# Optimization experiments

Measured on AMD Instinct MI355X. Metric: run time of the kernel, lower is better.

## Reference

```python
import jax
jax.config.update("jax_enable_x64", True)
import jax.numpy as jnp
import numpy as np

CKA_WEIGHT = 0.1


def _group_cka_sum(feats):
    """feats: [F, N, D] float. Returns sum of pairwise CKA over all (i,j) pairs.

    Faithful to CKASR: K = X X^T with zeroed diagonal, unbiased HSIC
    (Song et al. estimator), CKA[i,j] = HSIC(Ki,Kj)/sqrt(HSIC(Ki,Ki)HSIC(Kj,Kj)).
    All pairwise loops are batched into einsums.
    """
    F, N, D = feats.shape
    X = feats.reshape(F, N, D).astype(jnp.float64)
    K = jnp.einsum('fnd,fmd->fnm', X, X)                 # [F,N,N] Gram
    K = K * (1.0 - jnp.eye(N, dtype=K.dtype))            # fill_diagonal_(0)
    # HSIC(Ki, Kj) = 1/(N(N-3)) * ( tr(Ki Kj)
    #   + sum(Ki) sum(Kj) / ((N-1)(N-2))
    #   - 2/(N-2) * <rowsum(Ki), rowsum(Kj)> )
    trKL = jnp.einsum('iab,jab->ij', K, K)               # tr(Ki Kj), K symmetric
    s = jnp.sum(K, axis=(1, 2))                          # [F] total sums
    r = jnp.sum(K, axis=2)                               # [F,N] row sums
    rr = jnp.einsum('ia,ja->ij', r, r)                   # [F,F]
    hsic = (trKL + jnp.outer(s, s) / ((N - 1) * (N - 2))
            - 2.0 * rr / (N - 2)) / (N * (N - 3))        # [F,F]
    d = jnp.sqrt(jnp.diagonal(hsic))                     # [F]
    cka = hsic / (d[:, None] * d[None, :])
    return jnp.sum(cka)


def setup_inputs() -> dict:
    key = jax.random.key(0)
    k1, k2, k3, k4 = jax.random.split(key, 4)
    N, C = 64, 1000
    output = jax.random.normal(k1, (N, C), dtype=jnp.float32)
    target = jax.random.randint(k2, (N,), 0, C, dtype=jnp.int64)
    feats_a = jax.random.normal(k3, (3, N, 65536), dtype=jnp.float32)
    feats_b = jax.random.normal(k4, (4, N, 32768), dtype=jnp.float32)
    return {"output": output, "target": target,
            "feats_a": feats_a, "feats_b": feats_b}


def reference(output, target, feats_a, feats_b):
    N = output.shape[0]
    logp = jax.nn.log_softmax(output.astype(jnp.float32), axis=-1)
    ce = -jnp.mean(logp[jnp.arange(N), target])           # CrossEntropyLoss (mean)
    cka = _group_cka_sum(feats_a) + _group_cka_sum(feats_b)
    loss = ce + CKA_WEIGHT * cka.astype(jnp.float32)
    return (loss, output)
```

## Files before the change

### kernel.cpp

```cpp
#include <hip/hip_runtime.h>
#include <hip/hip_bf16.h>
#include <math.h>

typedef __attribute__((ext_vector_type(8))) short short8;
typedef __attribute__((ext_vector_type(4))) float f32x4;

#define PSTRIDE 4160

__device__ __forceinline__ unsigned int bf16_rn(float x) {
    unsigned int u = __float_as_uint(x);
    return (u + 0x7FFFu + ((u >> 16) & 1u)) >> 16;
}

__global__ __launch_bounds__(256) void ce_kernel(
    const float* __restrict__ logits, const int* __restrict__ target,
    float* __restrict__ out_copy, float* __restrict__ ce_rows)
{
    const int row = blockIdx.x;
    const float* x = logits + row * 1000;
    const int t = threadIdx.x;
    __shared__ float red[256];

    float m = -INFINITY;
    for (int i = t; i < 1000; i += 256) {
        float v = x[i];
        out_copy[row * 1000 + i] = v;
        m = fmaxf(m, v);
    }
    red[t] = m; __syncthreads();
    for (int s = 128; s > 0; s >>= 1) {
        if (t < s) red[t] = fmaxf(red[t], red[t + s]);
        __syncthreads();
    }
    m = red[0];
    __syncthreads();

    float ssum = 0.f;
    for (int i = t; i < 1000; i += 256) ssum += expf(x[i] - m);
    red[t] = ssum; __syncthreads();
    for (int s = 128; s > 0; s >>= 1) {
        if (t < s) red[t] += red[t + s];
        __syncthreads();
    }
    if (t == 0) {
        double lse = (double)m + log((double)red[0]);
        int tg = target[row];
        ce_rows[row] = (float)(-((double)x[tg] - lse));
    }
}

__global__ __launch_bounds__(256) void gramf_kernel(
    const float* __restrict__ A, const float* __restrict__ B,
    float* __restrict__ partials, int nfA, int nfB)
{
    __shared__ f32x4 ldsv[4096];
    char* lds = (char*)ldsv;

    const int blk = blockIdx.x;
    const int uA = nfA * 128;
    const float* xf;
    int c, D;
    if (blk < uA) {
        int f = blk >> 7; c = blk & 127; D = 65536;
        xf = A + (size_t)f * 64 * 65536;
    } else {
        int v = blk - uA;
        int f = v >> 6; c = v & 63; D = 32768;
        xf = B + (size_t)f * 64 * 32768;
    }

    const int t = threadIdx.x;
    const int wave = t >> 6, lane = t & 63;
    const int k0 = c * 512;

#pragma unroll 4
    for (int rr = 0; rr < 16; ++rr) {
        const int row = wave * 16 + rr;
        const float* p = xf + (size_t)row * D + k0 + lane * 8;
        float4 va = *(const float4*)p;
        float4 vb = *(const float4*)(p + 4);
        float vv[8] = {va.x, va.y, va.z, va.w, vb.x, vb.y, vb.z, vb.w};
        short8 hv;
#pragma unroll
        for (int j = 0; j < 8; ++j) hv[j] = (short)bf16_rn(vv[j]);
        const int boff = (lane * 16) ^ ((row & 7) << 4);
        *(short8*)(lds + row * 1024 + boff) = hv;
    }
    __syncthreads();

    const int m = lane & 15, quad = lane >> 4;
    const int loff = wave * 256 + quad * 16;

    f32x4 acc[4][4];
#pragma unroll
    for (int i = 0; i < 4; ++i)
#pragma unroll
        for (int j = 0; j < 4; ++j) acc[i][j] = (f32x4)0.f;

    short8 fr[4][4];
#pragma unroll
    for (int s = 0; s < 4; ++s)
#pragma unroll
        for (int tm = 0; tm < 4; ++tm) {
            const int row = tm * 16 + m;
            const int boff = (loff + s * 64) ^ ((row & 7) << 4);
            fr[s][tm] = *(const short8*)(lds + row * 1024 + boff);
        }
#pragma unroll
    for (int s = 0; s < 4; ++s)
#pragma unroll
        for (int tm = 0; tm < 4; ++tm)
#pragma unroll
            for (int tn = 0; tn < 4; ++tn)
                acc[tm][tn] = __builtin_amdgcn_mfma_f32_16x16x32_bf16(
                    fr[s][tm], fr[s][tn], acc[tm][tn], 0, 0, 0);

    __syncthreads();
    float* kbuf = (float*)lds;
    if (wave == 0) {
#pragma unroll
        for (int tm = 0; tm < 4; ++tm)
#pragma unroll
            for (int tn = 0; tn < 4; ++tn)
#pragma unroll
                for (int r = 0; r < 4; ++r)
                    kbuf[(tm * 16 + quad * 4 + r) * 64 + tn * 16 + m] = acc[tm][tn][r];
    }
    __syncthreads();
    if (wave != 0) {
#pragma unroll
        for (int tm = 0; tm < 4; ++tm)
#pragma unroll
            for (int tn = 0; tn < 4; ++tn)
#pragma unroll
                for (int r = 0; r < 4; ++r)
                    atomicAdd(&kbuf[(tm * 16 + quad * 4 + r) * 64 + tn * 16 + m],
                              acc[tm][tn][r]);
    }
    __syncthreads();

    float4* outp = (float4*)(partials + (size_t)blk * PSTRIDE);
    const float4* kb4 = (const float4*)kbuf;
    for (int e = t; e < 1024; e += 256) outp[e] = kb4[e];
}

__global__ __launch_bounds__(256) void reduce_kernel(
    const float* __restrict__ partials, float* __restrict__ K, int singleF)
{
    __shared__ double red[256];
    int f, eblk, base, count;
    if (singleF < 0) {
        f = blockIdx.x >> 6; eblk = blockIdx.x & 63;
        if (f < 3) { base = f * 128;            count = 128; }
        else       { base = 384 + (f - 3) * 64; count = 64;  }
    } else {
        f = singleF; eblk = blockIdx.x; base = 0;
        count = (f < 3) ? 128 : 64;
    }
    const int e = (eblk << 6) + (threadIdx.x & 63);
    const int jg = threadIdx.x >> 6;

    double s0 = 0.0, s1 = 0.0;
    for (int j = jg; j < count; j += 8) {
        s0 += (double)partials[(size_t)(base + j) * PSTRIDE + e];
        s1 += (double)partials[(size_t)(base + j + 4) * PSTRIDE + e];
    }
    red[threadIdx.x] = s0 + s1;
    __syncthreads();
    if (jg == 0) {
        double tot = red[threadIdx.x] + red[threadIdx.x + 64]
                   + red[threadIdx.x + 128] + red[threadIdx.x + 192];
        int rr = e >> 6, cc = e & 63;
        K[f * 4096 + e] = (rr == cc) ? 0.f : (float)tot;
    }
}

__global__ __launch_bounds__(256) void hsic_kernel(
    const float* __restrict__ K, double* __restrict__ hsic_out)
{
    const int p = blockIdx.x;
    int i, j;
    if (p < 9) { i = p / 3; j = p % 3; }
    else       { int q = p - 9; i = 3 + q / 4; j = 3 + q % 4; }
    const float* Ki = K + i * 4096;
    const float* Kj = K + j * 4096;
    const int t = threadIdx.x;

    __shared__ double red[256];
    __shared__ double ri[64], rj[64];

    double local = 0.0;
    for (int e = t; e < 4096; e += 256)
        local += (double)Ki[e] * (double)Kj[e];
    red[t] = local; __syncthreads();
    for (int s = 128; s > 0; s >>= 1) {
        if (t < s) red[t] += red[t + s];
        __syncthreads();
    }

    if (t < 64) {
        double s = 0.0;
        for (int mc = 0; mc < 64; ++mc) s += (double)Ki[t * 64 + mc];
        ri[t] = s;
    } else if (t < 128) {
        int n = t - 64;
        double s = 0.0;
        for (int mc = 0; mc < 64; ++mc) s += (double)Kj[n * 64 + mc];
        rj[n] = s;
    }
    __syncthreads();

    if (t == 0) {
        double tr = red[0];
        double rr = 0.0, si = 0.0, sj = 0.0;
        for (int n = 0; n < 64; ++n) {
            rr += ri[n] * rj[n];
            si += ri[n];
            sj += rj[n];
        }
        const double N = 64.0;
        const double c1 = (N - 1.0) * (N - 2.0);
        const double c2 = N - 2.0;
        const double c3 = N * (N - 3.0);
        hsic_out[p] = (tr + si * sj / c1 - 2.0 * rr / c2) / c3;
    }
}

__global__ __launch_bounds__(64) void final_kernel(
    const double* __restrict__ hsic, const float* __restrict__ ce_rows,
    float* __restrict__ out_loss)
{
    if (threadIdx.x != 0) return;
    double ce = 0.0;
    for (int n = 0; n < 64; ++n) ce += (double)ce_rows[n];
    ce /= 64.0;

    double cka_total = 0.0;
    for (int i = 0; i < 3; ++i)
        for (int j = 0; j < 3; ++j)
            cka_total += hsic[i * 3 + j] / sqrt(hsic[i * 3 + i] * hsic[j * 3 + j]);
    for (int i = 0; i < 4; ++i)
        for (int j = 0; j < 4; ++j)
            cka_total += hsic[9 + i * 4 + j] / sqrt(hsic[9 + i * 4 + i] * hsic[9 + j * 4 + j]);

    out_loss[0] = (float)(ce + 0.1 * cka_total);
}

extern "C" void kernel_launch(void* const* d_in, const int* in_sizes, int n_in,
                              void* d_out, int out_size, void* d_ws, size_t ws_size,
                              hipStream_t stream)
{
    const float* output  = (const float*)d_in[0];
    const int*   target  = (const int*)d_in[1];
    const float* feats_a = (const float*)d_in[2];
    const float* feats_b = (const float*)d_in[3];
    float* out = (float*)d_out;

    char* ws = (char*)d_ws;
    float*  K       = (float*)ws;
    float*  ce_rows = (float*)(ws + 114688);
    double* hsic    = (double*)(ws + 114944);
    float*  partials = (float*)(ws + 131072);

    const size_t partMain = (size_t)640 * PSTRIDE * 4;
    const size_t mainNeed = 131072 + partMain;

    hipLaunchKernelGGL(ce_kernel, dim3(64), dim3(256), 0, stream,
                       output, target, out + 1, ce_rows);

    if (ws_size >= mainNeed) {
        hipLaunchKernelGGL(gramf_kernel, dim3(640), dim3(256), 0, stream,
                           feats_a, feats_b, partials, 3, 4);
        hipLaunchKernelGGL(reduce_kernel, dim3(448), dim3(256), 0, stream,
                           partials, K, -1);
    } else {
        for (int f = 0; f < 7; ++f) {
            if (f < 3) {
                const float* X = feats_a + (size_t)f * 64 * 65536;
                hipLaunchKernelGGL(gramf_kernel, dim3(128), dim3(256), 0, stream,
                                   X, (const float*)nullptr, partials, 1, 0);
            } else {
                const float* X = feats_b + (size_t)(f - 3) * 64 * 32768;
                hipLaunchKernelGGL(gramf_kernel, dim3(64), dim3(256), 0, stream,
                                   (const float*)nullptr, X, partials, 0, 1);
            }
            hipLaunchKernelGGL(reduce_kernel, dim3(64), dim3(256), 0, stream,
                               partials, K, f);
        }
    }

    hipLaunchKernelGGL(hsic_kernel, dim3(25), dim3(256), 0, stream, K, hsic);
    hipLaunchKernelGGL(final_kernel, dim3(1), dim3(64), 0, stream,
                       hsic, ce_rows, out);
}
```

Before: 182.1 us.

## Fuse CE into gram kernel, drop LDS staging, merge HSIC and final kernels

```diff
diff --git a/kernel.cpp b/kernel.cpp
--- a/kernel.cpp
+++ b/kernel.cpp
@@ -1,9 +1,9 @@
 #include <hip/hip_runtime.h>
-#include <hip/hip_bf16.h>
 #include <math.h>
 
 typedef __attribute__((ext_vector_type(8))) short short8;
 typedef __attribute__((ext_vector_type(4))) float f32x4;
+typedef __attribute__((ext_vector_type(16))) float f32x16;
 
 #define PSTRIDE 4160
 
@@ -12,136 +12,124 @@
     return (u + 0x7FFFu + ((u >> 16) & 1u)) >> 16;
 }
 
-__global__ __launch_bounds__(256) void ce_kernel(
+__device__ __forceinline__ short8 cvt8(float4 a, float4 b) {
+    short8 h;
+    h[0] = (short)bf16_rn(a.x); h[1] = (short)bf16_rn(a.y);
+    h[2] = (short)bf16_rn(a.z); h[3] = (short)bf16_rn(a.w);
+    h[4] = (short)bf16_rn(b.x); h[5] = (short)bf16_rn(b.y);
+    h[6] = (short)bf16_rn(b.z); h[7] = (short)bf16_rn(b.w);
+    return h;
+}
+
+__global__ __launch_bounds__(512, 6) void gram_ce_kernel(
+    const float* __restrict__ A, const float* __restrict__ B,
+    float* __restrict__ partials, int nfA, int nfB,
     const float* __restrict__ logits, const int* __restrict__ target,
-    float* __restrict__ out_copy, float* __restrict__ ce_rows)
-{
-    const int row = blockIdx.x;
-    const float* x = logits + row * 1000;
+    float* __restrict__ out_copy, float* __restrict__ ce_rows, int ceCount)
+{
+    __shared__ float smem[4096];
     const int t = threadIdx.x;
-    __shared__ float red[256];
-
-    float m = -INFINITY;
-    for (int i = t; i < 1000; i += 256) {
-        float v = x[i];
-        out_copy[row * 1000 + i] = v;
-        m = fmaxf(m, v);
-    }
-    red[t] = m; __syncthreads();
-    for (int s = 128; s > 0; s >>= 1) {
-        if (t < s) red[t] = fmaxf(red[t], red[t + s]);
-        __syncthreads();
-    }
-    m = red[0];
-    __syncthreads();
-
-    float ssum = 0.f;
-    for (int i = t; i < 1000; i += 256) ssum += expf(x[i] - m);
-    red[t] = ssum; __syncthreads();
-    for (int s = 128; s > 0; s >>= 1) {
-        if (t < s) red[t] += red[t + s];
-        __syncthreads();
-    }
-    if (t == 0) {
-        double lse = (double)m + log((double)red[0]);
-        int tg = target[row];
-        ce_rows[row] = (float)(-((double)x[tg] - lse));
-    }
-}
-
-__global__ __launch_bounds__(256) void gramf_kernel(
-    const float* __restrict__ A, const float* __restrict__ B,
-    float* __restrict__ partials, int nfA, int nfB)
-{
-    __shared__ f32x4 ldsv[4096];
-    char* lds = (char*)ldsv;
-
-    const int blk = blockIdx.x;
+
+    if ((int)blockIdx.x < ceCount) {
+        const int row = blockIdx.x;
+        const float* x = logits + row * 1000;
+        float m = -INFINITY;
+        for (int i = t; i < 1000; i += 512) {
+            float v = x[i];
+            out_copy[row * 1000 + i] = v;
+            m = fmaxf(m, v);
+        }
+        smem[t] = m; __syncthreads();
+        for (int s = 256; s > 0; s >>= 1) {
+            if (t < s) smem[t] = fmaxf(smem[t], smem[t + s]);
+            __syncthreads();
+        }
+        m = smem[0];
+        __syncthreads();
+        float ssum = 0.f;
+        for (int i = t; i < 1000; i += 512) ssum += expf(x[i] - m);
+        smem[t] = ssum; __syncthreads();
+        for (int s = 256; s > 0; s >>= 1) {
+            if (t < s) smem[t] += smem[t + s];
+            __syncthreads();
+        }
+        if (t == 0) {
+            double lse = (double)m + log((double)smem[0]);
+            int tg = target[row];
+            ce_rows[row] = (float)(-((double)x[tg] - lse));
+        }
+        return;
+    }
+
+    const int gb = blockIdx.x - ceCount;
     const int uA = nfA * 128;
     const float* xf;
     int c, D;
-    if (blk < uA) {
-        int f = blk >> 7; c = blk & 127; D = 65536;
+    if (gb < uA) {
+        int f = gb >> 7; c = gb & 127; D = 65536;
         xf = A + (size_t)f * 64 * 65536;
     } else {
-        int v = blk - uA;
+        int v = gb - uA;
         int f = v >> 6; c = v & 63; D = 32768;
         xf = B + (size_t)f * 64 * 32768;
     }
 
-    const int t = threadIdx.x;
     const int wave = t >> 6, lane = t & 63;
-    const int k0 = c * 512;
-
-#pragma unroll 4
-    for (int rr = 0; rr < 16; ++rr) {
-        const int row = wave * 16 + rr;
-        const float* p = xf + (size_t)row * D + k0 + lane * 8;
-        float4 va = *(const float4*)p;
-        float4 vb = *(const float4*)(p + 4);
-        float vv[8] = {va.x, va.y, va.z, va.w, vb.x, vb.y, vb.z, vb.w};
-        short8 hv;
-#pragma unroll
-        for (int j = 0; j < 8; ++j) hv[j] = (short)bf16_rn(vv[j]);
-        const int boff = (lane * 16) ^ ((row & 7) << 4);
-        *(short8*)(lds + row * 1024 + boff) = hv;
-    }
-    __syncthreads();
-
-    const int m = lane & 15, quad = lane >> 4;
-    const int loff = wave * 256 + quad * 16;
-
-    f32x4 acc[4][4];
-#pragma unroll
-    for (int i = 0; i < 4; ++i)
-#pragma unroll
-        for (int j = 0; j < 4; ++j) acc[i][j] = (f32x4)0.f;
-
-    short8 fr[4][4];
-#pragma unroll
-    for (int s = 0; s < 4; ++s)
-#pragma unroll
-        for (int tm = 0; tm < 4; ++tm) {
-            const int row = tm * 16 + m;
-            const int boff = (loff + s * 64) ^ ((row & 7) << 4);
-            fr[s][tm] = *(const short8*)(lds + row * 1024 + boff);
-        }
-#pragma unroll
-    for (int s = 0; s < 4; ++s)
-#pragma unroll
-        for (int tm = 0; tm < 4; ++tm)
-#pragma unroll
-            for (int tn = 0; tn < 4; ++tn)
-                acc[tm][tn] = __builtin_amdgcn_mfma_f32_16x16x32_bf16(
-                    fr[s][tm], fr[s][tn], acc[tm][tn], 0, 0, 0);
-
-    __syncthreads();
-    float* kbuf = (float*)lds;
-    if (wave == 0) {
-#pragma unroll
-        for (int tm = 0; tm < 4; ++tm)
-#pragma unroll
-            for (int tn = 0; tn < 4; ++tn)
-#pragma unroll
-                for (int r = 0; r < 4; ++r)
-                    kbuf[(tm * 16 + quad * 4 + r) * 64 + tn * 16 + m] = acc[tm][tn][r];
-    }
-    __syncthreads();
-    if (wave != 0) {
-#pragma unroll
-        for (int tm = 0; tm < 4; ++tm)
-#pragma unroll
-            for (int tn = 0; tn < 4; ++tn)
-#pragma unroll
-                for (int r = 0; r < 4; ++r)
-                    atomicAdd(&kbuf[(tm * 16 + quad * 4 + r) * 64 + tn * 16 + m],
-                              acc[tm][tn][r]);
-    }
-    __syncthreads();
-
-    float4* outp = (float4*)(partials + (size_t)blk * PSTRIDE);
-    const float4* kb4 = (const float4*)kbuf;
-    for (int e = t; e < 1024; e += 256) outp[e] = kb4[e];
+    const int q = wave & 3, h = wave >> 2;
+    const int wr = q >> 1, wc = q & 1;
+    const int lr = lane & 31, hi = lane >> 5;
+    const int k0 = c * 512 + h * 256 + hi * 8;
+
+    const float* pA = xf + (size_t)(wr * 32 + lr) * D + k0;
+    const float* pB = xf + (size_t)(wc * 32 + lr) * D + k0;
+
+    f32x16 acc = (f32x16)0.f;
+    if (wr == wc) {
+#pragma unroll
+        for (int s = 0; s < 16; ++s) {
+            float4 a0 = *(const float4*)(pA + s * 16);
+            float4 a1 = *(const float4*)(pA + s * 16 + 4);
+            short8 fa = cvt8(a0, a1);
+            acc = __builtin_amdgcn_mfma_f32_32x32x16_bf16(fa, fa, acc, 0, 0, 0);
+        }
+    } else {
+#pragma unroll
+        for (int s = 0; s < 16; ++s) {
+            float4 a0 = *(const float4*)(pA + s * 16);
+            float4 a1 = *(const float4*)(pA + s * 16 + 4);
+            float4 b0 = *(const float4*)(pB + s * 16);
+            float4 b1 = *(const float4*)(pB + s * 16 + 4);
+            short8 fa = cvt8(a0, a1);
+            short8 fb = cvt8(b0, b1);
+            acc = __builtin_amdgcn_mfma_f32_32x32x16_bf16(fa, fb, acc, 0, 0, 0);
+        }
+    }
+
+    float* qb = smem + q * 1024;
+    if (h == 0) {
+#pragma unroll
+        for (int r = 0; r < 16; ++r) {
+            int rl = (r & 3) + 8 * (r >> 2) + 4 * hi;
+            qb[rl * 32 + lr] = acc[r];
+        }
+    }
+    __syncthreads();
+    if (h == 1) {
+#pragma unroll
+        for (int r = 0; r < 16; ++r) {
+            int rl = (r & 3) + 8 * (r >> 2) + 4 * hi;
+            qb[rl * 32 + lr] += acc[r];
+        }
+    }
+    __syncthreads();
+
+    float* outp = partials + (size_t)gb * PSTRIDE;
+    const f32x4* s4 = (const f32x4*)smem;
+    f32x4* o4 = (f32x4*)outp;
+    for (int e = t; e < 1024; e += 512) {
+        int qq = e >> 8, rl = (e >> 3) & 31, cl = e & 7;
+        o4[((qq >> 1) * 32 + rl) * 16 + (qq & 1) * 8 + cl] = s4[e];
+    }
 }
 
 __global__ __launch_bounds__(256) void reduce_kernel(
@@ -175,75 +163,73 @@
     }
 }
 
-__global__ __launch_bounds__(256) void hsic_kernel(
-    const float* __restrict__ K, double* __restrict__ hsic_out)
-{
-    const int p = blockIdx.x;
-    int i, j;
-    if (p < 9) { i = p / 3; j = p % 3; }
-    else       { int q = p - 9; i = 3 + q / 4; j = 3 + q % 4; }
-    const float* Ki = K + i * 4096;
-    const float* Kj = K + j * 4096;
+__global__ __launch_bounds__(256) void cka_final_kernel(
+    const float* __restrict__ K, const float* __restrict__ ce_rows,
+    float* __restrict__ out_loss)
+{
+    __shared__ double rs[448];
+    __shared__ double sf[8];
+    __shared__ double red[256];
+    __shared__ double hs[25];
     const int t = threadIdx.x;
 
-    __shared__ double red[256];
-    __shared__ double ri[64], rj[64];
-
-    double local = 0.0;
-    for (int e = t; e < 4096; e += 256)
-        local += (double)Ki[e] * (double)Kj[e];
-    red[t] = local; __syncthreads();
-    for (int s = 128; s > 0; s >>= 1) {
-        if (t < s) red[t] += red[t + s];
-        __syncthreads();
-    }
-
-    if (t < 64) {
+    for (int g = t; g < 448; g += 256) {
         double s = 0.0;
-        for (int mc = 0; mc < 64; ++mc) s += (double)Ki[t * 64 + mc];
-        ri[t] = s;
-    } else if (t < 128) {
-        int n = t - 64;
+        const float* kr = K + g * 64;
+        for (int c2 = 0; c2 < 64; ++c2) s += (double)kr[c2];
+        rs[g] = s;
+    }
+    __syncthreads();
+    if (t < 7) {
         double s = 0.0;
-        for (int mc = 0; mc < 64; ++mc) s += (double)Kj[n * 64 + mc];
-        rj[n] = s;
-    }
-    __syncthreads();
+        for (int r = 0; r < 64; ++r) s += rs[t * 64 + r];
+        sf[t] = s;
+    }
+    __syncthreads();
+
+    for (int p = 0; p < 25; ++p) {
+        int i, j;
+        if (p < 9) { i = p / 3; j = p % 3; }
+        else       { int qq = p - 9; i = 3 + qq / 4; j = 3 + qq % 4; }
+        const float* Ki = K + i * 4096;
+        const float* Kj = K + j * 4096;
+        double local = 0.0;
+        for (int e = t; e < 4096; e += 256)
+            local += (double)Ki[e] * (double)Kj[e];
+        red[t] = local; __syncthreads();
+        for (int s = 128; s > 0; s >>= 1) {
+            if (t < s) red[t] += red[t + s];
+            __syncthreads();
+        }
+        double tr = red[0];
+        __syncthreads();
+        red[t] = (t < 64) ? rs[i * 64 + t] * rs[j * 64 + t] : 0.0;
+        __syncthreads();
+        for (int s = 128; s > 0; s >>= 1) {
+            if (t < s) red[t] += red[t + s];
+            __syncthreads();
+        }
+        if (t == 0) {
+            const double N = 64.0;
+            hs[p] = (tr + sf[i] * sf[j] / ((N - 1.0) * (N - 2.0))
+                     - 2.0 * red[0] / (N - 2.0)) / (N * (N - 3.0));
+        }
+        __syncthreads();
+    }
 
     if (t == 0) {
-        double tr = red[0];
-        double rr = 0.0, si = 0.0, sj = 0.0;
-        for (int n = 0; n < 64; ++n) {
-            rr += ri[n] * rj[n];
-            si += ri[n];
-            sj += rj[n];
-        }
-        const double N = 64.0;
-        const double c1 = (N - 1.0) * (N - 2.0);
-        const double c2 = N - 2.0;
-        const double c3 = N * (N - 3.0);
-        hsic_out[p] = (tr + si * sj / c1 - 2.0 * rr / c2) / c3;
-    }
-}
-
-__global__ __launch_bounds__(64) void final_kernel(
-    const double* __restrict__ hsic, const float* __restrict__ ce_rows,
-    float* __restrict__ out_loss)
-{
-    if (threadIdx.x != 0) return;
-    double ce = 0.0;
-    for (int n = 0; n < 64; ++n) ce += (double)ce_rows[n];
-    ce /= 64.0;
-
-    double cka_total = 0.0;
-    for (int i = 0; i < 3; ++i)
-        for (int j = 0; j < 3; ++j)
-            cka_total += hsic[i * 3 + j] / sqrt(hsic[i * 3 + i] * hsic[j * 3 + j]);
-    for (int i = 0; i < 4; ++i)
-        for (int j = 0; j < 4; ++j)
-            cka_total += hsic[9 + i * 4 + j] / sqrt(hsic[9 + i * 4 + i] * hsic[9 + j * 4 + j]);
-
-    out_loss[0] = (float)(ce + 0.1 * cka_total);
+        double ce = 0.0;
+        for (int n = 0; n < 64; ++n) ce += (double)ce_rows[n];
+        ce /= 64.0;
+        double cka = 0.0;
+        for (int i = 0; i < 3; ++i)
+            for (int j = 0; j < 3; ++j)
+                cka += hs[i * 3 + j] / sqrt(hs[i * 3 + i] * hs[j * 3 + j]);
+        for (int i = 0; i < 4; ++i)
+            for (int j = 0; j < 4; ++j)
+                cka += hs[9 + i * 4 + j] / sqrt(hs[9 + i * 4 + i] * hs[9 + j * 4 + j]);
+        out_loss[0] = (float)(ce + 0.1 * cka);
+    }
 }
 
 extern "C" void kernel_launch(void* const* d_in, const int* in_sizes, int n_in,
@@ -257,39 +243,38 @@
     float* out = (float*)d_out;
 
     char* ws = (char*)d_ws;
-    float*  K       = (float*)ws;
-    float*  ce_rows = (float*)(ws + 114688);
-    double* hsic    = (double*)(ws + 114944);
+    float*  K        = (float*)ws;
+    float*  ce_rows  = (float*)(ws + 114688);
     float*  partials = (float*)(ws + 131072);
 
     const size_t partMain = (size_t)640 * PSTRIDE * 4;
     const size_t mainNeed = 131072 + partMain;
 
-    hipLaunchKernelGGL(ce_kernel, dim3(64), dim3(256), 0, stream,
-                       output, target, out + 1, ce_rows);
-
     if (ws_size >= mainNeed) {
-        hipLaunchKernelGGL(gramf_kernel, dim3(640), dim3(256), 0, stream,
-                           feats_a, feats_b, partials, 3, 4);
+        hipLaunchKernelGGL(gram_ce_kernel, dim3(640 + 64), dim3(512), 0, stream,
+                           feats_a, feats_b, partials, 3, 4,
+                           output, target, out + 1, ce_rows, 64);
         hipLaunchKernelGGL(reduce_kernel, dim3(448), dim3(256), 0, stream,
                            partials, K, -1);
     } else {
         for (int f = 0; f < 7; ++f) {
             if (f < 3) {
                 const float* X = feats_a + (size_t)f * 64 * 65536;
-                hipLaunchKernelGGL(gramf_kernel, dim3(128), dim3(256), 0, stream,
-                                   X, (const float*)nullptr, partials, 1, 0);
+                int ce = (f == 0) ? 64 : 0;
+                hipLaunchKernelGGL(gram_ce_kernel, dim3(128 + ce), dim3(512), 0, stream,
+                                   X, (const float*)nullptr, partials, 1, 0,
+                                   output, target, out + 1, ce_rows, ce);
             } else {
                 const float* X = feats_b + (size_t)(f - 3) * 64 * 32768;
-                hipLaunchKernelGGL(gramf_kernel, dim3(64), dim3(256), 0, stream,
-                                   (const float*)nullptr, X, partials, 0, 1);
+                hipLaunchKernelGGL(gram_ce_kernel, dim3(64), dim3(512), 0, stream,
+                                   (const float*)nullptr, X, partials, 0, 1,
+                                   output, target, out + 1, ce_rows, 0);
             }
             hipLaunchKernelGGL(reduce_kernel, dim3(64), dim3(256), 0, stream,
                                partials, K, f);
         }
     }
 
-    hipLaunchKernelGGL(hsic_kernel, dim3(25), dim3(256), 0, stream, K, hsic);
-    hipLaunchKernelGGL(final_kernel, dim3(1), dim3(64), 0, stream,
-                       hsic, ce_rows, out);
-}
+    hipLaunchKernelGGL(cka_final_kernel, dim3(1), dim3(256), 0, stream,
+                       K, ce_rows, out);
+}
```

New measurement: 227.8 us. +25.1%, slower.
